# Kernel tuning notes

Measured on AMD Instinct MI355X. Metric: run time of the kernel, lower is better.

Reference implementation:

```python
import jax, jax.numpy as jnp
import numpy as np

N_NODES = 50000
N_EDGES = 800000
C_IN = 64
N_HEADS = 4
HEAD_DIM = 16
FC = 64


def setup_inputs() -> dict:
    key = jax.random.key(0)
    ks = jax.random.split(key, 20)
    d = {}
    d["node_input"] = jax.random.normal(ks[0], (N_NODES, C_IN), jnp.float32)
    d["node_attr"] = jnp.ones((N_NODES, 1), jnp.float32)
    d["edge_src"] = jax.random.randint(ks[1], (N_EDGES,), 0, N_NODES)
    d["edge_dst"] = jax.random.randint(ks[2], (N_EDGES,), 0, N_NODES)
    d["edge_attr"] = jax.random.normal(ks[3], (N_EDGES, 1), jnp.float32)
    d["edge_scalars"] = jax.random.normal(ks[4], (N_EDGES, FC), jnp.float32)
    d["batch"] = jnp.zeros((N_NODES,), jnp.int32)
    s = 1.0 / np.sqrt(C_IN)
    AD = N_HEADS * HEAD_DIM  # 64
    d["Wq"] = jax.random.normal(ks[5], (C_IN, AD), jnp.float32) * s
    d["bq"] = jnp.zeros((AD,), jnp.float32)
    d["W_src"] = jax.random.normal(ks[6], (C_IN, C_IN), jnp.float32) * s
    d["b_src"] = jnp.zeros((C_IN,), jnp.float32)
    d["W_dst"] = jax.random.normal(ks[7], (C_IN, C_IN), jnp.float32) * s
    d["W_fc1"] = jax.random.normal(ks[8], (FC, FC), jnp.float32) * (1.0 / np.sqrt(FC))
    d["b_fc1"] = jnp.zeros((FC,), jnp.float32)
    d["W_fc2"] = jax.random.normal(ks[9], (FC, FC), jnp.float32) * (1.0 / np.sqrt(FC))
    d["b_fc2"] = jnp.zeros((FC,), jnp.float32)
    d["W_fc3"] = jax.random.normal(ks[10], (FC, C_IN), jnp.float32) * (1.0 / np.sqrt(FC))
    d["b_fc3"] = jnp.zeros((C_IN,), jnp.float32)
    d["W_kv"] = jax.random.normal(ks[11], (C_IN, 2 * AD), jnp.float32) * s
    d["b_kv"] = jnp.zeros((2 * AD,), jnp.float32)
    d["W_proj"] = jax.random.normal(ks[12], (AD, C_IN), jnp.float32) * (1.0 / np.sqrt(AD))
    d["b_proj"] = jnp.zeros((C_IN,), jnp.float32)
    return d


def reference(node_input, node_attr, edge_src, edge_dst, edge_attr, edge_scalars, batch,
              Wq, bq, W_src, b_src, W_dst, W_fc1, b_fc1, W_fc2, b_fc2, W_fc3, b_fc3,
              W_kv, b_kv, W_proj, b_proj):
    N = node_input.shape[0]
    # query: linear -> heads -> scale (ScaleFactor for HxH 0e irreps = 1/sqrt(num_irreps))
    q = (node_input @ Wq + bq).reshape(N, N_HEADS, HEAD_DIM)
    q = q * (1.0 / jnp.sqrt(jnp.float32(HEAD_DIM)))
    # edge messages
    msg_src = node_input @ W_src + b_src
    msg_dst = node_input @ W_dst
    kv = msg_src[edge_src] + msg_dst[edge_dst]  # [E, C]
    # SeparableFCTP (scalar irreps): radial MLP -> depthwise weights, x * edge_attr, linear
    h = jax.nn.silu(edge_scalars @ W_fc1 + b_fc1)
    h = jax.nn.silu(h @ W_fc2 + b_fc2)
    w = h @ W_fc3 + b_fc3  # [E, C] depthwise TP weights
    tp = kv * edge_attr * w
    kv2 = (tp @ W_kv + b_kv).reshape(-1, 2 * N_HEADS, HEAD_DIM)
    k = kv2[:, :N_HEADS]
    v = kv2[:, N_HEADS:]
    # per-edge scores and segment softmax over incoming edges of each dst node
    alpha = jnp.einsum('ehd,ehd->eh', q[edge_dst], k)  # [E, H]
    seg_max = jax.ops.segment_max(alpha, edge_dst, num_segments=N)
    seg_max = jnp.where(jnp.isfinite(seg_max), seg_max, 0.0)
    ex = jnp.exp(alpha - seg_max[edge_dst])
    denom = jax.ops.segment_sum(ex, edge_dst, num_segments=N)
    alpha = ex / (denom[edge_dst] + 1e-16)
    # weighted scatter-sum of values
    attn = jax.ops.segment_sum(v * alpha[..., None], edge_dst, num_segments=N)
    attn = attn.reshape(N, N_HEADS * HEAD_DIM)
    return attn @ W_proj + b_proj
```

## Files before the change

kernel.cpp:

```cpp
#include <hip/hip_runtime.h>
#include <hip/hip_bf16.h>


typedef __attribute__((ext_vector_type(8))) short    bf16x8;
typedef __attribute__((ext_vector_type(4))) float    f32x4;
typedef __attribute__((ext_vector_type(4))) unsigned short ushort4v;

__device__ __forceinline__ unsigned short f2bf(float x) {
    union { float f; unsigned u; } v; v.f = x;
    unsigned r = v.u + 0x7fffu + ((v.u >> 16) & 1u);
    return (unsigned short)(r >> 16);
}

__device__ __forceinline__ int swz(int row, int k) {
    return row * 64 + (k ^ ((row & 7) << 3));
}

__device__ __forceinline__ bf16x8 ldfrag(const unsigned short* buf, int rn, int kk, int lhi) {
    return *(const bf16x8*)(buf + swz(rn, kk * 32 + lhi * 8));
}

#define PHASE_FENCE() asm volatile("" ::: "memory")

__global__ __launch_bounds__(256)
void prep_weights(const float* __restrict__ W1, const float* __restrict__ W2,
                  const float* __restrict__ W3, const float* __restrict__ Wkv,
                  unsigned short* __restrict__ wbf)
{
    const int d = blockIdx.x * 256 + threadIdx.x;
    if (d < 12288) {
        const int w  = d >> 12;
        const int r  = d & 4095;
        const int n  = r >> 6, kx = r & 63;
        const int k  = kx ^ ((n & 7) << 3);
        const float* W = (w == 0) ? W1 : (w == 1) ? W2 : W3;
        wbf[d] = f2bf(W[k * 64 + n]);
    } else if (d < 20480) {
        const int r  = d - 12288;
        const int n  = r >> 6, kx = r & 63;
        const int k  = kx ^ ((n & 7) << 3);
        wbf[d] = f2bf(Wkv[k * 128 + n]);
    }
}

__global__ __launch_bounds__(384)
void node_linear_kernel(const float* __restrict__ x,
                        const float* __restrict__ Wq,   const float* __restrict__ bq,
                        const float* __restrict__ Wsrc, const float* __restrict__ bsrc,
                        const float* __restrict__ Wdst,
                        float* __restrict__ qout, float* __restrict__ msout,
                        float* __restrict__ mdout, int N, int ntiles)
{
    __shared__ __align__(16) float sW[64 * 192];
    __shared__ float sb[192];
    __shared__ __align__(16) float xs[32][68];

    const int t = threadIdx.x;
    for (int idx4 = t; idx4 < 3072; idx4 += 384) {
        const int k  = idx4 / 48;
        const int j4 = idx4 % 48;
        const float4* src = (j4 < 16) ? (const float4*)&Wq  [k * 64 + j4 * 4]
                         : (j4 < 32) ? (const float4*)&Wsrc[k * 64 + (j4 - 16) * 4]
                                     : (const float4*)&Wdst[k * 64 + (j4 - 32) * 4];
        ((float4*)sW)[idx4] = *src;
    }
    if (t < 192) sb[t] = (t < 64) ? bq[t] : (t < 128) ? bsrc[t - 64] : 0.0f;

    const int te = t / 48, tj = t % 48;
    const int j0 = tj * 4, e0 = te * 4;

    for (int tile = blockIdx.x; tile < ntiles; tile += gridDim.x) {
        const int nbase = tile * 32;
        __syncthreads();
        for (int idx = t; idx < 512; idx += 384) {
            const int n  = idx >> 4;
            const int c4 = (idx & 15) * 4;
            const int gn = nbase + n;
            float4 g = make_float4(0.f, 0.f, 0.f, 0.f);
            if (gn < N) g = *(const float4*)&x[(size_t)gn * 64 + c4];
            *(float4*)&xs[n][c4] = g;
        }
        __syncthreads();

        float acc[4][4];
#pragma unroll
        for (int i = 0; i < 4; ++i)
#pragma unroll
            for (int c = 0; c < 4; ++c) acc[i][c] = 0.f;

#pragma unroll 16
        for (int k = 0; k < 64; ++k) {
            const float4 wv = *(const float4*)&sW[k * 192 + j0];
            const float a0 = xs[e0 + 0][k], a1 = xs[e0 + 1][k];
            const float a2 = xs[e0 + 2][k], a3 = xs[e0 + 3][k];
            acc[0][0] += a0 * wv.x; acc[0][1] += a0 * wv.y; acc[0][2] += a0 * wv.z; acc[0][3] += a0 * wv.w;
            acc[1][0] += a1 * wv.x; acc[1][1] += a1 * wv.y; acc[1][2] += a1 * wv.z; acc[1][3] += a1 * wv.w;
            acc[2][0] += a2 * wv.x; acc[2][1] += a2 * wv.y; acc[2][2] += a2 * wv.z; acc[2][3] += a2 * wv.w;
            acc[3][0] += a3 * wv.x; acc[3][1] += a3 * wv.y; acc[3][2] += a3 * wv.z; acc[3][3] += a3 * wv.w;
        }

#pragma unroll
        for (int i = 0; i < 4; ++i) {
            const int gn = nbase + e0 + i;
            if (gn >= N) continue;
            float4 o;
            o.x = acc[i][0] + sb[j0 + 0];
            o.y = acc[i][1] + sb[j0 + 1];
            o.z = acc[i][2] + sb[j0 + 2];
            o.w = acc[i][3] + sb[j0 + 3];
            if (j0 < 64) {
                o.x *= 0.25f; o.y *= 0.25f; o.z *= 0.25f; o.w *= 0.25f;
                *(float4*)&qout[(size_t)gn * 64 + j0] = o;
            } else if (j0 < 128) {
                *(float4*)&msout[(size_t)gn * 64 + (j0 - 64)] = o;
            } else {
                *(float4*)&mdout[(size_t)gn * 64 + (j0 - 128)] = o;
            }
        }
    }
}

__global__ __launch_bounds__(512, 4)
void edge_fused_mfma(const int* __restrict__ esrc, const int* __restrict__ edst,
                     const float* __restrict__ eattr, const float* __restrict__ escal,
                     const unsigned short* __restrict__ wbf,
                     const float* __restrict__ b1, const float* __restrict__ b2,
                     const float* __restrict__ b3, const float* __restrict__ bkv,
                     const float* __restrict__ qbuf, const float* __restrict__ msrc,
                     const float* __restrict__ mdst,
                     float* __restrict__ num, float* __restrict__ den, int ntiles)
{
    __shared__ __align__(16) unsigned short sh[36864];
    unsigned short* sW1t  = sh;
    unsigned short* sW2t  = sh + 4096;
    unsigned short* sW3t  = sh + 8192;
    unsigned short* sWkvt = sh + 12288;
    unsigned short* sA0   = sh + 20480;
    unsigned short* sA1   = sh + 28672;
    __shared__ float sB1[64], sB2[64], sB3[64], sBkv[128];

    const int t    = threadIdx.x;
    const int lane = t & 63;
    const int wave = t >> 6;
    const int l15  = lane & 15;
    const int lhi  = lane >> 4;
    const int rowBase = wave * 16;
    const int r4   = lhi * 4;

    for (int i4 = t; i4 < 2560; i4 += 512)
        ((float4*)sh)[i4] = ((const float4*)wbf)[i4];
    if (t < 64)              { sB1[t] = b1[t]; sB2[t] = b2[t]; sB3[t] = b3[t]; }
    if (t >= 64 && t < 192)  sBkv[t - 64] = bkv[t - 64];
    __syncthreads();

    const int srow = lane >> 4;
    const int scol = (lane & 15) << 2;

    for (int tile = blockIdx.x; tile < ntiles; tile += gridDim.x) {
        const int base  = tile * 128;
        const int ebase = base + rowBase;

#pragma unroll
        for (int p = 0; p < 4; ++p) {
            const int row = p * 4 + srow;
            const float4 g = *(const float4*)&escal[(size_t)(ebase + row) * 64 + scol];
            ushort4v pk = { f2bf(g.x), f2bf(g.y), f2bf(g.z), f2bf(g.w) };
            *(ushort4v*)&sA0[swz(rowBase + row, scol)] = pk;
        }

        int   gsrc[4], gdst[4];
        float gea[4];
#pragma unroll
        for (int r = 0; r < 4; ++r) {
            const int e = ebase + r4 + r;
            gsrc[r] = esrc[e];
            gdst[r] = edst[e];
            gea[r]  = eattr[e];
        }
        float qreg[4][4];
#pragma unroll
        for (int h = 0; h < 4; ++h)
#pragma unroll
            for (int r = 0; r < 4; ++r)
                qreg[h][r] = qbuf[(size_t)gdst[r] * 64 + h * 16 + l15];

        PHASE_FENCE();

        {
            f32x4 acc[4] = {{0,0,0,0},{0,0,0,0},{0,0,0,0},{0,0,0,0}};
#pragma unroll
            for (int kk = 0; kk < 2; ++kk) {
                const bf16x8 a = ldfrag(sA0, rowBase + l15, kk, lhi);
#pragma unroll
                for (int c = 0; c < 4; ++c) {
                    const bf16x8 b = ldfrag(sW1t, c * 16 + l15, kk, lhi);
                    acc[c] = __builtin_amdgcn_mfma_f32_16x16x32_bf16(a, b, acc[c], 0, 0, 0);
                }
            }
#pragma unroll
            for (int c = 0; c < 4; ++c)
#pragma unroll
                for (int r = 0; r < 4; ++r) {
                    const int row = rowBase + r4 + r;
                    const int col = c * 16 + l15;
                    const float v = acc[c][r] + sB1[col];
                    sA1[swz(row, col)] = f2bf(v / (1.f + __expf(-v)));
                }
        }
        PHASE_FENCE();

        {
            f32x4 acc[4] = {{0,0,0,0},{0,0,0,0},{0,0,0,0},{0,0,0,0}};
#pragma unroll
            for (int kk = 0; kk < 2; ++kk) {
                const bf16x8 a = ldfrag(sA1, rowBase + l15, kk, lhi);
#pragma unroll
                for (int c = 0; c < 4; ++c) {
                    const bf16x8 b = ldfrag(sW2t, c * 16 + l15, kk, lhi);
                    acc[c] = __builtin_amdgcn_mfma_f32_16x16x32_bf16(a, b, acc[c], 0, 0, 0);
                }
            }
#pragma unroll
            for (int c = 0; c < 4; ++c)
#pragma unroll
                for (int r = 0; r < 4; ++r) {
                    const int row = rowBase + r4 + r;
                    const int col = c * 16 + l15;
                    const float v = acc[c][r] + sB2[col];
                    sA0[swz(row, col)] = f2bf(v / (1.f + __expf(-v)));
                }
        }
        PHASE_FENCE();

        {
            f32x4 acc[4] = {{0,0,0,0},{0,0,0,0},{0,0,0,0},{0,0,0,0}};
#pragma unroll
            for (int kk = 0; kk < 2; ++kk) {
                const bf16x8 a = ldfrag(sA0, rowBase + l15, kk, lhi);
#pragma unroll
                for (int c = 0; c < 4; ++c) {
                    const bf16x8 b = ldfrag(sW3t, c * 16 + l15, kk, lhi);
                    acc[c] = __builtin_amdgcn_mfma_f32_16x16x32_bf16(a, b, acc[c], 0, 0, 0);
                }
            }
            float ms[4][4], md[4][4];
#pragma unroll
            for (int c = 0; c < 4; ++c)
#pragma unroll
                for (int r = 0; r < 4; ++r) {
                    const int col = c * 16 + l15;
                    ms[c][r] = msrc[(size_t)gsrc[r] * 64 + col];
                    md[c][r] = mdst[(size_t)gdst[r] * 64 + col];
                }
#pragma unroll
            for (int c = 0; c < 4; ++c)
#pragma unroll
                for (int r = 0; r < 4; ++r) {
                    const int row = rowBase + r4 + r;
                    const int col = c * 16 + l15;
                    const float w  = acc[c][r] + sB3[col];
                    const float tp = (ms[c][r] + md[c][r]) * gea[r] * w;
                    sA1[swz(row, col)] = f2bf(tp);
                }
        }
        PHASE_FENCE();

        f32x4 acc2[8] = {{0,0,0,0},{0,0,0,0},{0,0,0,0},{0,0,0,0},
                         {0,0,0,0},{0,0,0,0},{0,0,0,0},{0,0,0,0}};
#pragma unroll
        for (int kk = 0; kk < 2; ++kk) {
            const bf16x8 a = ldfrag(sA1, rowBase + l15, kk, lhi);
#pragma unroll
            for (int c = 0; c < 8; ++c) {
                const bf16x8 b = ldfrag(sWkvt, c * 16 + l15, kk, lhi);
                acc2[c] = __builtin_amdgcn_mfma_f32_16x16x32_bf16(a, b, acc2[c], 0, 0, 0);
            }
        }

        float ex[4][4];
#pragma unroll
        for (int h = 0; h < 4; ++h)
#pragma unroll
            for (int r = 0; r < 4; ++r) {
                float s = (acc2[h][r] + sBkv[h * 16 + l15]) * qreg[h][r];
                s += __shfl_xor(s, 1);
                s += __shfl_xor(s, 2);
                s += __shfl_xor(s, 4);
                s += __shfl_xor(s, 8);
                const float e = __expf(s);
                ex[h][r] = e;
                if (l15 == h * 4 + r) atomicAdd(&den[(size_t)gdst[r] * 4 + h], e);
            }

#pragma unroll
        for (int vt = 0; vt < 4; ++vt)
#pragma unroll
            for (int r = 0; r < 4; ++r) {
                const float vv = acc2[4 + vt][r] + sBkv[64 + vt * 16 + l15];
                atomicAdd(&num[(size_t)gdst[r] * 64 + vt * 16 + l15], ex[vt][r] * vv);
            }

        PHASE_FENCE();
    }
}

__global__ __launch_bounds__(256)
void final_proj_kernel(const float* __restrict__ num, const float* __restrict__ den,
                       const float* __restrict__ Wp, const float* __restrict__ bp,
                       float* __restrict__ out, int N, int ntiles)
{
    __shared__ __align__(16) float sW[64 * 64];
    __shared__ float sb[64];
    __shared__ __align__(16) float at[64][68];

    const int t = threadIdx.x;
    for (int i4 = t; i4 < 1024; i4 += 256)
        ((float4*)sW)[i4] = ((const float4*)Wp)[i4];
    if (t < 64) sb[t] = bp[t];

    const int te = t >> 4, tj = t & 15;
    const int j0 = tj * 4, e0 = te * 4;

    for (int tile = blockIdx.x; tile < ntiles; tile += gridDim.x) {
        const int nbase = tile * 64;
        __syncthreads();
        for (int idx = t; idx < 1024; idx += 256) {
            const int n  = idx >> 4;
            const int c4 = (idx & 15) * 4;
            const int gn = nbase + n;
            float4 g = make_float4(0.f, 0.f, 0.f, 0.f);
            if (gn < N) {
                const float4 nm = *(const float4*)&num[(size_t)gn * 64 + c4];
                const float inv = 1.0f / (den[(size_t)gn * 4 + (c4 >> 4)] + 1e-16f);
                g = make_float4(nm.x * inv, nm.y * inv, nm.z * inv, nm.w * inv);
            }
            *(float4*)&at[n][c4] = g;
        }
        __syncthreads();

        float acc[4][4];
#pragma unroll
        for (int i = 0; i < 4; ++i)
#pragma unroll
            for (int c = 0; c < 4; ++c) acc[i][c] = 0.f;

#pragma unroll 16
        for (int k = 0; k < 64; ++k) {
            const float4 wv = *(const float4*)&sW[k * 64 + j0];
            const float a0 = at[e0 + 0][k], a1 = at[e0 + 1][k];
            const float a2 = at[e0 + 2][k], a3 = at[e0 + 3][k];
            acc[0][0] += a0 * wv.x; acc[0][1] += a0 * wv.y; acc[0][2] += a0 * wv.z; acc[0][3] += a0 * wv.w;
            acc[1][0] += a1 * wv.x; acc[1][1] += a1 * wv.y; acc[1][2] += a1 * wv.z; acc[1][3] += a1 * wv.w;
            acc[2][0] += a2 * wv.x; acc[2][1] += a2 * wv.y; acc[2][2] += a2 * wv.z; acc[2][3] += a2 * wv.w;
            acc[3][0] += a3 * wv.x; acc[3][1] += a3 * wv.y; acc[3][2] += a3 * wv.z; acc[3][3] += a3 * wv.w;
        }

#pragma unroll
        for (int i = 0; i < 4; ++i) {
            const int gn = nbase + e0 + i;
            if (gn >= N) continue;
            float4 o;
            o.x = acc[i][0] + sb[j0 + 0];
            o.y = acc[i][1] + sb[j0 + 1];
            o.z = acc[i][2] + sb[j0 + 2];
            o.w = acc[i][3] + sb[j0 + 3];
            *(float4*)&out[(size_t)gn * 64 + j0] = o;
        }
    }
}

extern "C" void kernel_launch(void* const* d_in, const int* in_sizes, int n_in,
                              void* d_out, int out_size, void* d_ws, size_t ws_size,
                              hipStream_t stream)
{
    const float* node_input = (const float*)d_in[0];
    const int*   edge_src   = (const int*)  d_in[2];
    const int*   edge_dst   = (const int*)  d_in[3];
    const float* edge_attr  = (const float*)d_in[4];
    const float* edge_scal  = (const float*)d_in[5];
    const float* Wq    = (const float*)d_in[7];
    const float* bq    = (const float*)d_in[8];
    const float* W_src = (const float*)d_in[9];
    const float* b_src = (const float*)d_in[10];
    const float* W_dst = (const float*)d_in[11];
    const float* W_fc1 = (const float*)d_in[12];
    const float* b_fc1 = (const float*)d_in[13];
    const float* W_fc2 = (const float*)d_in[14];
    const float* b_fc2 = (const float*)d_in[15];
    const float* W_fc3 = (const float*)d_in[16];
    const float* b_fc3 = (const float*)d_in[17];
    const float* W_kv  = (const float*)d_in[18];
    const float* b_kv  = (const float*)d_in[19];
    const float* W_proj = (const float*)d_in[20];
    const float* b_proj = (const float*)d_in[21];

    const int N = in_sizes[0] / 64;
    const int E = in_sizes[2];

    float* ws    = (float*)d_ws;
    float* q_buf = ws;
    float* msrc  = ws + (size_t)N * 64;
    float* mdst  = ws + (size_t)N * 128;
    float* num   = ws + (size_t)N * 192;
    float* den   = ws + (size_t)N * 256;
    unsigned short* wbf = (unsigned short*)(ws + (size_t)N * 260);

    hipMemsetAsync(num, 0, (size_t)N * 68 * sizeof(float), stream);

    prep_weights<<<80, 256, 0, stream>>>(W_fc1, W_fc2, W_fc3, W_kv, wbf);

    {
        const int ntiles = (N + 31) / 32;
        node_linear_kernel<<<512, 384, 0, stream>>>(node_input, Wq, bq, W_src, b_src, W_dst,
                                                    q_buf, msrc, mdst, N, ntiles);
    }
    {
        const int ntiles = E / 128;
        edge_fused_mfma<<<512, 512, 0, stream>>>(edge_src, edge_dst, edge_attr, edge_scal,
                                                 wbf, b_fc1, b_fc2, b_fc3, b_kv,
                                                 q_buf, msrc, mdst, num, den, ntiles);
    }
    {
        const int ntiles = (N + 63) / 64;
        final_proj_kernel<<<512, 256, 0, stream>>>(num, den, W_proj, b_proj,
                                                   (float*)d_out, N, ntiles);
    }
}
```

Measured before the change: 672.0 us.

## Sort edges by destination via counting sort and coalesce scatter atomics

Adds a histogram, single-block scan and atomic ranking pass that builds a permutation grouping edges by destination node. The edge kernel then processes edges in that order and merges consecutive same-destination contributions within each lane's four rows before issuing atomics to num and den. The goal is fewer atomic operations and better locality for the q and num accesses. In exchange it adds three extra kernel launches, a serial single-block scan over 50k nodes, and indirect gathers of edge_scalars and edge indices through perm.

```diff
diff --git a/kernel.cpp b/kernel.cpp
--- a/kernel.cpp
+++ b/kernel.cpp
@@ -21,6 +21,55 @@
 }
 
 #define PHASE_FENCE() asm volatile("" ::: "memory")
+
+__global__ __launch_bounds__(256)
+void hist_kernel(const int* __restrict__ edst, int* __restrict__ cnt, int E)
+{
+    const int e = blockIdx.x * 256 + threadIdx.x;
+    if (e < E) atomicAdd(&cnt[edst[e]], 1);
+}
+
+__global__ __launch_bounds__(1024)
+void scan_kernel(const int* __restrict__ cnt, int* __restrict__ cursor, int N)
+{
+    __shared__ int wsum[16];
+    const int t = threadIdx.x;
+    const int lane = t & 63, wv = t >> 6;
+    const int CH = (N + 1023) / 1024;
+    const int lo = t * CH;
+    const int hi = (lo + CH < N) ? lo + CH : N;
+    int s = 0;
+    for (int i = lo; i < hi; ++i) s += cnt[i];
+    int x = s;
+    for (int off = 1; off < 64; off <<= 1) {
+        int y = __shfl_up(x, off);
+        if (lane >= off) x += y;
+    }
+    if (lane == 63) wsum[wv] = x;
+    __syncthreads();
+    if (wv == 0 && lane < 16) {
+        int w = wsum[lane];
+        for (int off = 1; off < 16; off <<= 1) {
+            int y = __shfl_up(w, off);
+            if (lane >= off) w += y;
+        }
+        wsum[lane] = w;
+    }
+    __syncthreads();
+    int base = (wv > 0 ? wsum[wv - 1] : 0) + (x - s);
+    for (int i = lo; i < hi; ++i) { cursor[i] = base; base += cnt[i]; }
+}
+
+__global__ __launch_bounds__(256)
+void rank_kernel(const int* __restrict__ edst, int* __restrict__ cursor,
+                 int* __restrict__ perm, int E)
+{
+    const int e = blockIdx.x * 256 + threadIdx.x;
+    if (e < E) {
+        const int p = atomicAdd(&cursor[edst[e]], 1);
+        perm[p] = e;
+    }
+}
 
 __global__ __launch_bounds__(256)
 void prep_weights(const float* __restrict__ W1, const float* __restrict__ W2,
@@ -123,6 +172,7 @@
 __global__ __launch_bounds__(512, 4)
 void edge_fused_mfma(const int* __restrict__ esrc, const int* __restrict__ edst,
                      const float* __restrict__ eattr, const float* __restrict__ escal,
+                     const int* __restrict__ perm,
                      const unsigned short* __restrict__ wbf,
                      const float* __restrict__ b1, const float* __restrict__ b2,
                      const float* __restrict__ b3, const float* __restrict__ bkv,
@@ -163,19 +213,21 @@
 #pragma unroll
         for (int p = 0; p < 4; ++p) {
             const int row = p * 4 + srow;
-            const float4 g = *(const float4*)&escal[(size_t)(ebase + row) * 64 + scol];
+            const int er  = perm[ebase + row];
+            const float4 g = *(const float4*)&escal[(size_t)er * 64 + scol];
             ushort4v pk = { f2bf(g.x), f2bf(g.y), f2bf(g.z), f2bf(g.w) };
             *(ushort4v*)&sA0[swz(rowBase + row, scol)] = pk;
         }
 
-        int   gsrc[4], gdst[4];
+        int   eids[4], gsrc[4], gdst[4];
         float gea[4];
 #pragma unroll
+        for (int r = 0; r < 4; ++r) eids[r] = perm[ebase + r4 + r];
+#pragma unroll
         for (int r = 0; r < 4; ++r) {
-            const int e = ebase + r4 + r;
-            gsrc[r] = esrc[e];
-            gdst[r] = edst[e];
-            gea[r]  = eattr[e];
+            gsrc[r] = esrc[eids[r]];
+            gdst[r] = edst[eids[r]];
+            gea[r]  = eattr[eids[r]];
         }
         float qreg[4][4];
 #pragma unroll
@@ -278,6 +330,7 @@
         }
 
         float ex[4][4];
+        float dh[4] = {0.f, 0.f, 0.f, 0.f};
 #pragma unroll
         for (int h = 0; h < 4; ++h)
 #pragma unroll
@@ -289,16 +342,33 @@
                 s += __shfl_xor(s, 8);
                 const float e = __expf(s);
                 ex[h][r] = e;
-                if (l15 == h * 4 + r) atomicAdd(&den[(size_t)gdst[r] * 4 + h], e);
-            }
-
-#pragma unroll
-        for (int vt = 0; vt < 4; ++vt)
+                if (l15 == h) dh[r] = e;
+            }
+
+        if (l15 < 4) {
+            float accd = 0.f;
 #pragma unroll
             for (int r = 0; r < 4; ++r) {
-                const float vv = acc2[4 + vt][r] + sBkv[64 + vt * 16 + l15];
-                atomicAdd(&num[(size_t)gdst[r] * 64 + vt * 16 + l15], ex[vt][r] * vv);
-            }
+                accd += dh[r];
+                if (r == 3 || gdst[r + 1] != gdst[r]) {
+                    atomicAdd(&den[(size_t)gdst[r] * 4 + l15], accd);
+                    accd = 0.f;
+                }
+            }
+        }
+
+#pragma unroll
+        for (int vt = 0; vt < 4; ++vt) {
+            float accv = 0.f;
+#pragma unroll
+            for (int r = 0; r < 4; ++r) {
+                accv += ex[vt][r] * (acc2[4 + vt][r] + sBkv[64 + vt * 16 + l15]);
+                if (r == 3 || gdst[r + 1] != gdst[r]) {
+                    atomicAdd(&num[(size_t)gdst[r] * 64 + vt * 16 + l15], accv);
+                    accv = 0.f;
+                }
+            }
+        }
 
         PHASE_FENCE();
     }
@@ -404,10 +474,18 @@
     float* num   = ws + (size_t)N * 192;
     float* den   = ws + (size_t)N * 256;
     unsigned short* wbf = (unsigned short*)(ws + (size_t)N * 260);
+    int* cnt    = (int*)(ws + (size_t)N * 260 + 10240);
+    int* cursor = cnt + N;
+    int* perm   = cursor + N;
 
     hipMemsetAsync(num, 0, (size_t)N * 68 * sizeof(float), stream);
+    hipMemsetAsync(cnt, 0, (size_t)N * sizeof(int), stream);
 
     prep_weights<<<80, 256, 0, stream>>>(W_fc1, W_fc2, W_fc3, W_kv, wbf);
+
+    hist_kernel<<<(E + 255) / 256, 256, 0, stream>>>(edge_dst, cnt, E);
+    scan_kernel<<<1, 1024, 0, stream>>>(cnt, cursor, N);
+    rank_kernel<<<(E + 255) / 256, 256, 0, stream>>>(edge_dst, cursor, perm, E);
 
     {
         const int ntiles = (N + 31) / 32;
@@ -417,7 +495,7 @@
     {
         const int ntiles = E / 128;
         edge_fused_mfma<<<512, 512, 0, stream>>>(edge_src, edge_dst, edge_attr, edge_scal,
-                                                 wbf, b_fc1, b_fc2, b_fc3, b_kv,
+                                                 perm, wbf, b_fc1, b_fc2, b_fc3, b_kv,
                                                  q_buf, msrc, mdst, num, den, ntiles);
     }
     {
```

Measured after the change: 694.2 us. 1.03x slower.
